# Performance work log

Measured on AMD Instinct MI355X. Metric: run time of the kernel, lower is better.

Reference implementation:

```python
import jax, jax.numpy as jnp
import numpy as np

H, DH = 8, 64          # num_heads, head_dim
DM = H * DH            # hidden_dim = 512
LAM = 1.0              # lambda_param
SCALE = 1.0 / np.sqrt(DH)


def setup_inputs() -> dict:
    key = jax.random.key(0)
    ks = jax.random.split(key, 12)
    B, N, R = 2, 2048, 16
    s = DM ** -0.5
    inp = {
        "x": jax.random.normal(ks[0], (B, N, DM), jnp.float32),
        "pde_residuals": jax.random.normal(ks[1], (B, N, R), jnp.float32),
        "mask": jnp.ones((B, 1, N, N), jnp.int32),
        "Wq": jax.random.normal(ks[2], (DM, DM), jnp.float32) * s,
        "bq": jax.random.normal(ks[3], (DM,), jnp.float32) * 0.01,
        "Wk": jax.random.normal(ks[4], (DM, DM), jnp.float32) * s,
        "bk": jax.random.normal(ks[5], (DM,), jnp.float32) * 0.01,
        "Wv": jax.random.normal(ks[6], (DM, DM), jnp.float32) * s,
        "bv": jax.random.normal(ks[7], (DM,), jnp.float32) * 0.01,
        "Wo": jax.random.normal(ks[8], (DM, DM), jnp.float32) * s,
        "bo": jax.random.normal(ks[9], (DM,), jnp.float32) * 0.01,
    }
    return inp


def reference(x, pde_residuals, mask, Wq, bq, Wk, bk, Wv, bv, Wo, bo):
    B, N, _ = x.shape
    # torch nn.Linear: y = x @ W.T + b
    q = (x @ Wq.T + bq).reshape(B, N, H, DH)
    k = (x @ Wk.T + bk).reshape(B, N, H, DH)
    v = (x @ Wv.T + bv).reshape(B, N, H, DH)
    # [B,H,N,N]
    scores = jnp.einsum('bqhd,bkhd->bhqk', q, k) * SCALE
    # residual bias: rb.unsqueeze(1) - rb.unsqueeze(2) -> bias[b,i,j] = rb[b,j] - rb[b,i]
    rb = jnp.linalg.norm(pde_residuals, axis=-1)            # [B,N]
    bias = rb[:, None, None, :] - rb[:, None, :, None]       # [B,1,N,N]
    scores = scores - LAM * bias
    scores = jnp.where(mask == 0, -jnp.inf, scores)
    attn = jax.nn.softmax(scores, axis=-1)                   # dropout is identity in eval
    out = jnp.einsum('bhqk,bkhd->bqhd', attn, v).reshape(B, N, DM)
    return out @ Wo.T + bo
```

## Files before the change

### kernel.cpp

```cpp
#include <hip/hip_runtime.h>
#include <hip/hip_bf16.h>
#include <math.h>

#define B_ 2
#define N_ 2048
#define H_ 8
#define DH_ 64
#define DM_ 512
#define R_ 16
#define LAM_ 1.0f
#define SCALE_ 0.125f

typedef unsigned short u16;
typedef unsigned int u32;
typedef u16 u16x4 __attribute__((ext_vector_type(4)));
typedef u16 u16x8 __attribute__((ext_vector_type(8)));
typedef __bf16 bf16x8 __attribute__((ext_vector_type(8)));
typedef float f32x4 __attribute__((ext_vector_type(4)));

static __device__ __forceinline__ u16 f2bf(float f) {
    union { float f; unsigned u; } v; v.f = f;
    unsigned r = v.u + 0x7FFF + ((v.u >> 16) & 1);
    return (u16)(r >> 16);
}

static __device__ __forceinline__ u32 pack_bf16(float lo, float hi) {
    float2 f2; f2.x = lo; f2.y = hi;
    __hip_bfloat162 h2 = __float22bfloat162_rn(f2);
    u32 r;
    __builtin_memcpy(&r, &h2, 4);
    return r;
}

static __device__ __forceinline__ void gl_lds16(const void* g, void* l) {
    __builtin_amdgcn_global_load_lds(
        (const __attribute__((address_space(1))) unsigned*)g,
        (__attribute__((address_space(3))) unsigned*)l, 16, 0, 0);
}

__global__ __launch_bounds__(256) void cast_all(
    const float* __restrict__ x, const float* __restrict__ wq,
    const float* __restrict__ wk, const float* __restrict__ wv,
    const float* __restrict__ wo, u16* __restrict__ xb, u16* __restrict__ wqb,
    u16* __restrict__ wkb, u16* __restrict__ wvb, u16* __restrict__ wob) {
    int y = blockIdx.y;
    const float* src; u16* dst; int n;
    switch (y) {
        case 0: src = x;  dst = xb;  n = 2097152; break;
        case 1: src = wq; dst = wqb; n = 262144;  break;
        case 2: src = wk; dst = wkb; n = 262144;  break;
        case 3: src = wv; dst = wvb; n = 262144;  break;
        default: src = wo; dst = wob; n = 262144; break;
    }
    int i = (blockIdx.x * 256 + threadIdx.x) * 8;
    if (i >= n) return;
    float4 a = *(const float4*)(src + i);
    float4 b = *(const float4*)(src + i + 4);
    u16x8 o;
    o[0] = f2bf(a.x); o[1] = f2bf(a.y); o[2] = f2bf(a.z); o[3] = f2bf(a.w);
    o[4] = f2bf(b.x); o[5] = f2bf(b.y); o[6] = f2bf(b.z); o[7] = f2bf(b.w);
    *(u16x8*)(dst + i) = o;
}

__global__ void rb_kernel(const float* __restrict__ pde, float* __restrict__ rbs) {
    int i = blockIdx.x * blockDim.x + threadIdx.x;
    if (i >= B_ * N_) return;
    const float4* p = (const float4*)(pde + (size_t)i * R_);
    float s = 0.f;
#pragma unroll
    for (int j = 0; j < 4; ++j) {
        float4 v = p[j];
        s += v.x * v.x + v.y * v.y + v.z * v.z + v.w * v.w;
    }
    rbs[i] = LAM_ * sqrtf(s);
}

__global__ __launch_bounds__(256) void mask_scan(const int* __restrict__ mask,
                                                 int* __restrict__ flags) {
    int kt = blockIdx.x, qt = blockIdx.y, b = blockIdx.z;
    __shared__ int red;
    if (threadIdx.x == 0) red = 0;
    __syncthreads();
    int any = 0;
    for (int c = threadIdx.x; c < 1024; c += 256) {
        int row = c >> 4, seg = c & 15;
        int4 m4 = *(const int4*)(mask + (size_t)b * N_ * N_ +
                                 (size_t)(qt * 64 + row) * N_ + kt * 64 + seg * 4);
        any |= (m4.x == 0) | (m4.y == 0) | (m4.z == 0) | (m4.w == 0);
    }
    if (__ballot(any)) {
        if ((threadIdx.x & 63) == 0) atomicOr(&red, 1);
    }
    __syncthreads();
    if (threadIdx.x == 0) flags[(b * 32 + qt) * 32 + kt] = red;
}

struct Acc { f32x4 v[2][2]; };

static __device__ __forceinline__ Acc gemm_core(const u16* __restrict__ A,
                                                const u16* __restrict__ W,
                                                int m0, int nn0, char* LDSB) {
    int t = threadIdx.x, l = t & 63, w = t >> 6;
    int lg = l >> 4, li = l & 15;
    int wr = w >> 1, wc = w & 1;
    Acc acc;
#pragma unroll
    for (int m = 0; m < 2; ++m)
#pragma unroll
        for (int n = 0; n < 2; ++n) acc.v[m][n] = (f32x4){0.f, 0.f, 0.f, 0.f};

    int srow_l = l >> 3;
    int colb = ((l & 7) * 16) ^ (srow_l << 4);

    for (int k0 = 0; k0 < DM_; k0 += 64) {
        __syncthreads();
#pragma unroll
        for (int i = 0; i < 2; ++i) {
            int c = w * 2 + i;
            int row = c * 8 + srow_l;
            gl_lds16(A + (size_t)(m0 + row) * DM_ + k0 + (colb >> 1),
                     LDSB + c * 1024);
            gl_lds16(W + (size_t)(nn0 + row) * DM_ + k0 + (colb >> 1),
                     LDSB + 8192 + c * 1024);
        }
        __syncthreads();
#pragma unroll
        for (int kk = 0; kk < 2; ++kk) {
            bf16x8 af[2], bfr[2];
#pragma unroll
            for (int m = 0; m < 2; ++m) {
                int r = wr * 32 + m * 16 + li;
                af[m] = *(const bf16x8*)(LDSB + r * 128 +
                                         ((kk * 64 + lg * 16) ^ ((r & 7) << 4)));
            }
#pragma unroll
            for (int n = 0; n < 2; ++n) {
                int r = wc * 32 + n * 16 + li;
                bfr[n] = *(const bf16x8*)(LDSB + 8192 + r * 128 +
                                          ((kk * 64 + lg * 16) ^ ((r & 7) << 4)));
            }
#pragma unroll
            for (int m = 0; m < 2; ++m)
#pragma unroll
                for (int n = 0; n < 2; ++n)
                    acc.v[m][n] = __builtin_amdgcn_mfma_f32_16x16x32_bf16(
                        af[m], bfr[n], acc.v[m][n], 0, 0, 0);
        }
    }
    return acc;
}

__global__ __launch_bounds__(256) void gemm_qkv(
    const u16* __restrict__ xb, const u16* __restrict__ wqb,
    const u16* __restrict__ wkb, const u16* __restrict__ wvb,
    const float* __restrict__ bq, const float* __restrict__ bk,
    const float* __restrict__ bv, u16* __restrict__ q_bf,
    u16* __restrict__ k_bf, u16* __restrict__ vt) {
    __shared__ char LDSB[24576];
    int y = blockIdx.y;
    int which = y >> 3;
    int nn0 = (y & 7) * 64;
    const u16* W = which == 0 ? wqb : which == 1 ? wkb : wvb;
    const float* bias = which == 0 ? bq : which == 1 ? bk : bv;
    int m0 = blockIdx.x * 64;
    Acc acc = gemm_core(xb, W, m0, nn0, LDSB);

    int t = threadIdx.x, l = t & 63, w = t >> 6;
    int lg = l >> 4, li = l & 15;
    int wr = w >> 1, wc = w & 1;
    float scale = which == 0 ? SCALE_ : 1.0f;
#pragma unroll
    for (int n = 0; n < 2; ++n) {
        int col = nn0 + wc * 32 + n * 16 + li;
        float bv_ = bias[col];
        if (which < 2) {
            u16* dst = which == 0 ? q_bf : k_bf;
#pragma unroll
            for (int m = 0; m < 2; ++m)
#pragma unroll
                for (int r = 0; r < 4; ++r) {
                    int row = m0 + wr * 32 + m * 16 + lg * 4 + r;
                    dst[(size_t)row * DM_ + col] =
                        f2bf((acc.v[m][n][r] + bv_) * scale);
                }
        } else {
            int h = col >> 6, d = col & 63;
#pragma unroll
            for (int m = 0; m < 2; ++m) {
                int row = m0 + wr * 32 + m * 16 + lg * 4;
                int b = row >> 11, nb = row & (N_ - 1);
                u16x4 o;
#pragma unroll
                for (int r = 0; r < 4; ++r) o[r] = f2bf(acc.v[m][n][r] + bv_);
                *(u16x4*)(vt + ((size_t)((b * 8 + h) * 64 + d)) * N_ + nb) = o;
            }
        }
    }
}

__global__ __launch_bounds__(256) void gemm_out(
    const u16* __restrict__ aob, const u16* __restrict__ wob,
    const float* __restrict__ bo, float* __restrict__ out) {
    __shared__ char LDSB[24576];
    int nn0 = blockIdx.y * 64;
    int m0 = blockIdx.x * 64;
    Acc acc = gemm_core(aob, wob, m0, nn0, LDSB);

    int t = threadIdx.x, l = t & 63, w = t >> 6;
    int lg = l >> 4, li = l & 15;
    int wr = w >> 1, wc = w & 1;
#pragma unroll
    for (int n = 0; n < 2; ++n) {
        int col = nn0 + wc * 32 + n * 16 + li;
        float bv_ = bo[col];
#pragma unroll
        for (int m = 0; m < 2; ++m)
#pragma unroll
            for (int r = 0; r < 4; ++r) {
                int row = m0 + wr * 32 + m * 16 + lg * 4 + r;
                out[(size_t)row * DM_ + col] = acc.v[m][n][r] + bv_;
            }
    }
}

__global__ __launch_bounds__(512) void attn8(
    const u16* __restrict__ qb, const u16* __restrict__ kb,
    const u16* __restrict__ vtb, const float* __restrict__ rbs,
    const int* __restrict__ mask, const int* __restrict__ flags,
    u16* __restrict__ aob) {
    __shared__ char KVB[2][2][16384];
    __shared__ char PsB[8][2048];

    int t = threadIdx.x, l = t & 63, w = t >> 6;
    int g2 = w >> 2, wq = w & 3;
    int raw = blockIdx.x;
    int sid = (raw & 7) * 64 + (raw >> 3);
    int bh = sid >> 5, qg = sid & 31;
    int b = bh >> 3, h = bh & 7;
    int m0 = qg * 64 + wq * 16;
    int lg = l >> 4, li = l & 15;
    int k0base = g2 * 1024;

    int srl = l >> 3;
    int colb = ((l & 7) * 16) ^ (srl << 4);

    bf16x8 qa[2];
    {
        const u16* qrow = qb + (size_t)(b * N_ + m0 + li) * DM_ + h * DH_;
        qa[0] = __builtin_bit_cast(bf16x8, *(const u16x8*)(qrow + lg * 8));
        qa[1] = __builtin_bit_cast(bf16x8, *(const u16x8*)(qrow + 32 + lg * 8));
    }

    f32x4 o[4];
#pragma unroll
    for (int dt = 0; dt < 4; ++dt) o[dt] = (f32x4){0.f, 0.f, 0.f, 0.f};
    float mrun = -INFINITY, lrun = 0.f;

    auto STAGE = [&](int bufi, int k0s) {
        char* base = &KVB[g2][bufi][0];
#pragma unroll
        for (int c = 0; c < 2; ++c) {
            int chunk = wq * 2 + c;
            int row = chunk * 8 + srl;
            gl_lds16(kb + (size_t)(b * N_ + k0s + row) * DM_ + h * DH_ + (colb >> 1),
                     base + chunk * 1024);
            gl_lds16(vtb + ((size_t)(bh * DH_ + row)) * N_ + k0s + (colb >> 1),
                     base + 8192 + chunk * 1024);
        }
    };

    STAGE(0, k0base);
    __syncthreads();

    char* pwbase = &PsB[w][0] + li * 16 + ((lg & 1) << 3);
    int slot_lohi = (lg >> 1);

    int buf = 0;
    for (int tt = 0; tt < 16; ++tt) {
        int k0 = k0base + tt * 64;
        if (tt < 15) STAGE(buf ^ 1, k0 + 64);

        const char* Kb = &KVB[g2][buf][0];
        const char* Vb = &KVB[g2][buf][8192];
        int flag = flags[(b * 32 + qg) * 32 + (k0 >> 6)];

        f32x4 st[4];
        __builtin_amdgcn_s_setprio(1);
#pragma unroll
        for (int kt = 0; kt < 4; ++kt) {
            st[kt] = (f32x4){0.f, 0.f, 0.f, 0.f};
#pragma unroll
            for (int s = 0; s < 2; ++s) {
                int key = kt * 16 + li;
                bf16x8 kf = *(const bf16x8*)(Kb + key * 128 +
                                             ((s * 64 + lg * 16) ^ ((key & 7) << 4)));
                st[kt] = __builtin_amdgcn_mfma_f32_16x16x32_bf16(kf, qa[s], st[kt],
                                                                 0, 0, 0);
            }
        }
        __builtin_amdgcn_s_setprio(0);

#pragma unroll
        for (int kt = 0; kt < 4; ++kt) {
            float4 rb4 = *(const float4*)(rbs + b * N_ + k0 + kt * 16 + lg * 4);
            st[kt][0] -= rb4.x; st[kt][1] -= rb4.y;
            st[kt][2] -= rb4.z; st[kt][3] -= rb4.w;
        }
        if (flag) {
#pragma unroll
            for (int kt = 0; kt < 4; ++kt)
#pragma unroll
                for (int r = 0; r < 4; ++r) {
                    int rowg = m0 + li;
                    int keyg = k0 + kt * 16 + lg * 4 + r;
                    if (mask[(size_t)b * N_ * N_ + (size_t)rowg * N_ + keyg] == 0)
                        st[kt][r] = -INFINITY;
                }
        }

        float m0_ = fmaxf(fmaxf(st[0][0], st[0][1]), fmaxf(st[0][2], st[0][3]));
        float m1_ = fmaxf(fmaxf(st[1][0], st[1][1]), fmaxf(st[1][2], st[1][3]));
        float m2_ = fmaxf(fmaxf(st[2][0], st[2][1]), fmaxf(st[2][2], st[2][3]));
        float m3_ = fmaxf(fmaxf(st[3][0], st[3][1]), fmaxf(st[3][2], st[3][3]));
        float pmax = fmaxf(fmaxf(m0_, m1_), fmaxf(m2_, m3_));
        pmax = fmaxf(pmax, __shfl_xor(pmax, 16));
        pmax = fmaxf(pmax, __shfl_xor(pmax, 32));

        if (!__all(pmax - mrun <= 8.0f)) {
            float mnew = fmaxf(fmaxf(mrun, pmax), -3.0e38f);
            float corr = __expf(mrun - mnew);
            mrun = mnew;
            lrun *= corr;
#pragma unroll
            for (int dt = 0; dt < 4; ++dt)
#pragma unroll
                for (int r = 0; r < 4; ++r) o[dt][r] *= corr;
        }

        float ps[8];
#pragma unroll
        for (int kt = 0; kt < 4; ++kt) {
            float p0 = __expf(st[kt][0] - mrun);
            float p1 = __expf(st[kt][1] - mrun);
            float p2 = __expf(st[kt][2] - mrun);
            float p3 = __expf(st[kt][3] - mrun);
            ps[kt * 2 + 0] = p0 + p1;
            ps[kt * 2 + 1] = p2 + p3;
            uint2 pkw;
            pkw.x = pack_bf16(p0, p1);
            pkw.y = pack_bf16(p2, p3);
            int slot = (kt >> 1) * 4 + (kt & 1) * 2 + slot_lohi;
            *(uint2*)(pwbase + (slot << 8)) = pkw;
        }
        float psum = ((ps[0] + ps[1]) + (ps[2] + ps[3])) +
                     ((ps[4] + ps[5]) + (ps[6] + ps[7]));
        psum += __shfl_xor(psum, 16);
        psum += __shfl_xor(psum, 32);
        lrun += psum;

        bf16x8 pf[2];
#pragma unroll
        for (int s = 0; s < 2; ++s)
            pf[s] = *(const bf16x8*)(&PsB[w][0] + ((s * 4 + lg) << 8) + li * 16);
        __builtin_amdgcn_s_setprio(1);
#pragma unroll
        for (int dt = 0; dt < 4; ++dt)
#pragma unroll
            for (int s = 0; s < 2; ++s) {
                int d = dt * 16 + li;
                bf16x8 vf = *(const bf16x8*)(Vb + d * 128 +
                                             ((s * 64 + lg * 16) ^ ((d & 7) << 4)));
                o[dt] = __builtin_amdgcn_mfma_f32_16x16x32_bf16(vf, pf[s], o[dt],
                                                                0, 0, 0);
            }
        __builtin_amdgcn_s_setprio(0);

        __syncthreads();
        buf ^= 1;
    }

    float* cmb = (float*)&KVB[0][0][0];
    float* mlc = (float*)&PsB[0][0];
    if (g2 == 1) {
        float* dst = cmb + wq * 1024;
#pragma unroll
        for (int dt = 0; dt < 4; ++dt)
            *(f32x4*)(dst + li * 64 + dt * 16 + lg * 4) = o[dt];
        if (lg == 0) {
            float2 ml; ml.x = mrun; ml.y = lrun;
            *(float2*)(mlc + (wq * 16 + li) * 2) = ml;
        }
    }
    __syncthreads();
    if (g2 == 0) {
        float2 ml1 = *(const float2*)(mlc + (wq * 16 + li) * 2);
        float m = fmaxf(mrun, ml1.x);
        float w0 = __expf(mrun - m), w1 = __expf(ml1.x - m);
        float denom = 1.f / (lrun * w0 + ml1.y * w1);
        w0 *= denom; w1 *= denom;
        const float* src = cmb + wq * 1024;
        u16* orow = aob + (size_t)(b * N_ + m0 + li) * DM_ + h * DH_;
#pragma unroll
        for (int dt = 0; dt < 4; ++dt) {
            f32x4 p1 = *(const f32x4*)(src + li * 64 + dt * 16 + lg * 4);
            u16x4 ov;
#pragma unroll
            for (int r = 0; r < 4; ++r)
                ov[r] = f2bf(o[dt][r] * w0 + p1[r] * w1);
            *(u16x4*)(orow + dt * 16 + lg * 4) = ov;
        }
    }
}

extern "C" void kernel_launch(void* const* d_in, const int* in_sizes, int n_in,
                              void* d_out, int out_size, void* d_ws, size_t ws_size,
                              hipStream_t stream) {
    const float* x   = (const float*)d_in[0];
    const float* pde = (const float*)d_in[1];
    const int*   msk = (const int*)d_in[2];
    const float* Wq  = (const float*)d_in[3];
    const float* bq  = (const float*)d_in[4];
    const float* Wk  = (const float*)d_in[5];
    const float* bk  = (const float*)d_in[6];
    const float* Wv  = (const float*)d_in[7];
    const float* bv  = (const float*)d_in[8];
    const float* Wo  = (const float*)d_in[9];
    const float* bo  = (const float*)d_in[10];
    float* out = (float*)d_out;

    const size_t MAT = (size_t)B_ * N_ * DM_;
    const size_t WSZ = (size_t)DM_ * DM_;
    u16* xb   = (u16*)d_ws;
    u16* q_bf = xb + MAT;
    u16* k_bf = q_bf + MAT;
    u16* vt   = k_bf + MAT;
    u16* aob  = vt + MAT;
    u16* wqb  = aob + MAT;
    u16* wkb  = wqb + WSZ;
    u16* wvb  = wkb + WSZ;
    u16* wob  = wvb + WSZ;
    float* rbs = (float*)(wob + WSZ);
    int* flags = (int*)(rbs + B_ * N_);

    cast_all<<<dim3(1024, 5), 256, 0, stream>>>(x, Wq, Wk, Wv, Wo,
                                                xb, wqb, wkb, wvb, wob);
    rb_kernel<<<(B_ * N_ + 255) / 256, 256, 0, stream>>>(pde, rbs);
    mask_scan<<<dim3(32, 32, 2), 256, 0, stream>>>(msk, flags);

    gemm_qkv<<<dim3(64, 24), 256, 0, stream>>>(xb, wqb, wkb, wvb,
                                               bq, bk, bv, q_bf, k_bf, vt);

    attn8<<<512, 512, 0, stream>>>(q_bf, k_bf, vt, rbs, msk, flags, aob);

    gemm_out<<<dim3(64, 8), 256, 0, stream>>>(aob, wob, bo, out);
}
```

Measured before the change: 76.89 us.

## Halve attention key tile to 32 and defer row-sum reductions

```diff
diff --git a/kernel.cpp b/kernel.cpp
--- a/kernel.cpp
+++ b/kernel.cpp
@@ -223,13 +223,13 @@
     }
 }
 
-__global__ __launch_bounds__(512) void attn8(
+__global__ __launch_bounds__(512) void attn9(
     const u16* __restrict__ qb, const u16* __restrict__ kb,
     const u16* __restrict__ vtb, const float* __restrict__ rbs,
     const int* __restrict__ mask, const int* __restrict__ flags,
     u16* __restrict__ aob) {
-    __shared__ char KVB[2][2][16384];
-    __shared__ char PsB[8][2048];
+    __shared__ char KVB[2][2][8192];
+    __shared__ char PsB[8][1024];
 
     int t = threadIdx.x, l = t & 63, w = t >> 6;
     int g2 = w >> 2, wq = w & 3;
@@ -243,6 +243,7 @@
 
     int srl = l >> 3;
     int colb = ((l & 7) * 16) ^ (srl << 4);
+    int vsrc_u = (l & 7) ^ srl;
 
     bf16x8 qa[2];
     {
@@ -258,36 +259,34 @@
 
     auto STAGE = [&](int bufi, int k0s) {
         char* base = &KVB[g2][bufi][0];
-#pragma unroll
-        for (int c = 0; c < 2; ++c) {
-            int chunk = wq * 2 + c;
-            int row = chunk * 8 + srl;
-            gl_lds16(kb + (size_t)(b * N_ + k0s + row) * DM_ + h * DH_ + (colb >> 1),
-                     base + chunk * 1024);
-            gl_lds16(vtb + ((size_t)(bh * DH_ + row)) * N_ + k0s + (colb >> 1),
-                     base + 8192 + chunk * 1024);
-        }
+        int row = wq * 8 + srl;
+        gl_lds16(kb + (size_t)(b * N_ + k0s + row) * DM_ + h * DH_ + (colb >> 1),
+                 base + wq * 1024);
+        gl_lds16(vtb + ((size_t)(bh * DH_ + row * 2 + (vsrc_u >> 2))) * N_ +
+                     k0s + (vsrc_u & 3) * 8,
+                 base + 4096 + wq * 1024);
     };
 
     STAGE(0, k0base);
     __syncthreads();
 
     char* pwbase = &PsB[w][0] + li * 16 + ((lg & 1) << 3);
-    int slot_lohi = (lg >> 1);
+    int slot_lo = lg >> 1;
+    int vfoff = ((li & 1) * 64 + lg * 16) ^ ((li >> 1) << 4);
 
     int buf = 0;
-    for (int tt = 0; tt < 16; ++tt) {
-        int k0 = k0base + tt * 64;
-        if (tt < 15) STAGE(buf ^ 1, k0 + 64);
+    for (int tt = 0; tt < 32; ++tt) {
+        int k0 = k0base + tt * 32;
+        if (tt < 31) STAGE(buf ^ 1, k0 + 32);
 
         const char* Kb = &KVB[g2][buf][0];
-        const char* Vb = &KVB[g2][buf][8192];
+        const char* Vb = &KVB[g2][buf][4096];
         int flag = flags[(b * 32 + qg) * 32 + (k0 >> 6)];
 
-        f32x4 st[4];
+        f32x4 st[2];
         __builtin_amdgcn_s_setprio(1);
 #pragma unroll
-        for (int kt = 0; kt < 4; ++kt) {
+        for (int kt = 0; kt < 2; ++kt) {
             st[kt] = (f32x4){0.f, 0.f, 0.f, 0.f};
 #pragma unroll
             for (int s = 0; s < 2; ++s) {
@@ -301,14 +300,14 @@
         __builtin_amdgcn_s_setprio(0);
 
 #pragma unroll
-        for (int kt = 0; kt < 4; ++kt) {
+        for (int kt = 0; kt < 2; ++kt) {
             float4 rb4 = *(const float4*)(rbs + b * N_ + k0 + kt * 16 + lg * 4);
             st[kt][0] -= rb4.x; st[kt][1] -= rb4.y;
             st[kt][2] -= rb4.z; st[kt][3] -= rb4.w;
         }
         if (flag) {
 #pragma unroll
-            for (int kt = 0; kt < 4; ++kt)
+            for (int kt = 0; kt < 2; ++kt)
 #pragma unroll
                 for (int r = 0; r < 4; ++r) {
                     int rowg = m0 + li;
@@ -318,15 +317,13 @@
                 }
         }
 
-        float m0_ = fmaxf(fmaxf(st[0][0], st[0][1]), fmaxf(st[0][2], st[0][3]));
-        float m1_ = fmaxf(fmaxf(st[1][0], st[1][1]), fmaxf(st[1][2], st[1][3]));
-        float m2_ = fmaxf(fmaxf(st[2][0], st[2][1]), fmaxf(st[2][2], st[2][3]));
-        float m3_ = fmaxf(fmaxf(st[3][0], st[3][1]), fmaxf(st[3][2], st[3][3]));
-        float pmax = fmaxf(fmaxf(m0_, m1_), fmaxf(m2_, m3_));
-        pmax = fmaxf(pmax, __shfl_xor(pmax, 16));
-        pmax = fmaxf(pmax, __shfl_xor(pmax, 32));
-
-        if (!__all(pmax - mrun <= 8.0f)) {
+        float mymax = fmaxf(
+            fmaxf(fmaxf(st[0][0], st[0][1]), fmaxf(st[0][2], st[0][3])),
+            fmaxf(fmaxf(st[1][0], st[1][1]), fmaxf(st[1][2], st[1][3])));
+        if (!__all(mymax - mrun <= 8.0f)) {
+            float pmax = mymax;
+            pmax = fmaxf(pmax, __shfl_xor(pmax, 16));
+            pmax = fmaxf(pmax, __shfl_xor(pmax, 32));
             float mnew = fmaxf(fmaxf(mrun, pmax), -3.0e38f);
             float corr = __expf(mrun - mnew);
             mrun = mnew;
@@ -337,47 +334,35 @@
                 for (int r = 0; r < 4; ++r) o[dt][r] *= corr;
         }
 
-        float ps[8];
-#pragma unroll
-        for (int kt = 0; kt < 4; ++kt) {
+#pragma unroll
+        for (int kt = 0; kt < 2; ++kt) {
             float p0 = __expf(st[kt][0] - mrun);
             float p1 = __expf(st[kt][1] - mrun);
             float p2 = __expf(st[kt][2] - mrun);
             float p3 = __expf(st[kt][3] - mrun);
-            ps[kt * 2 + 0] = p0 + p1;
-            ps[kt * 2 + 1] = p2 + p3;
+            lrun += (p0 + p1) + (p2 + p3);
             uint2 pkw;
             pkw.x = pack_bf16(p0, p1);
             pkw.y = pack_bf16(p2, p3);
-            int slot = (kt >> 1) * 4 + (kt & 1) * 2 + slot_lohi;
-            *(uint2*)(pwbase + (slot << 8)) = pkw;
-        }
-        float psum = ((ps[0] + ps[1]) + (ps[2] + ps[3])) +
-                     ((ps[4] + ps[5]) + (ps[6] + ps[7]));
-        psum += __shfl_xor(psum, 16);
-        psum += __shfl_xor(psum, 32);
-        lrun += psum;
-
-        bf16x8 pf[2];
-#pragma unroll
-        for (int s = 0; s < 2; ++s)
-            pf[s] = *(const bf16x8*)(&PsB[w][0] + ((s * 4 + lg) << 8) + li * 16);
+            *(uint2*)(pwbase + ((kt * 2 + slot_lo) << 8)) = pkw;
+        }
+
+        bf16x8 pf = *(const bf16x8*)(&PsB[w][0] + (lg << 8) + li * 16);
         __builtin_amdgcn_s_setprio(1);
 #pragma unroll
-        for (int dt = 0; dt < 4; ++dt)
-#pragma unroll
-            for (int s = 0; s < 2; ++s) {
-                int d = dt * 16 + li;
-                bf16x8 vf = *(const bf16x8*)(Vb + d * 128 +
-                                             ((s * 64 + lg * 16) ^ ((d & 7) << 4)));
-                o[dt] = __builtin_amdgcn_mfma_f32_16x16x32_bf16(vf, pf[s], o[dt],
-                                                                0, 0, 0);
-            }
+        for (int dt = 0; dt < 4; ++dt) {
+            bf16x8 vf = *(const bf16x8*)(Vb + (dt * 8 + (li >> 1)) * 128 + vfoff);
+            o[dt] = __builtin_amdgcn_mfma_f32_16x16x32_bf16(vf, pf, o[dt],
+                                                            0, 0, 0);
+        }
         __builtin_amdgcn_s_setprio(0);
 
         __syncthreads();
         buf ^= 1;
     }
+
+    lrun += __shfl_xor(lrun, 16);
+    lrun += __shfl_xor(lrun, 32);
 
     float* cmb = (float*)&KVB[0][0][0];
     float* mlc = (float*)&PsB[0][0];
@@ -450,7 +435,7 @@
     gemm_qkv<<<dim3(64, 24), 256, 0, stream>>>(xb, wqb, wkb, wvb,
                                                bq, bk, bv, q_bf, k_bf, vt);
 
-    attn8<<<512, 512, 0, stream>>>(q_bf, k_bf, vt, rbs, msk, flags, aob);
+    attn9<<<512, 512, 0, stream>>>(q_bf, k_bf, vt, rbs, msk, flags, aob);
 
     gemm_out<<<dim3(64, 8), 256, 0, stream>>>(aob, wob, bo, out);
 }
```

New measurement: 82.62 us. +7.4%, slower.
